# Kernel tuning notes

Hardware: AMD Instinct MI355X
Metric: run time of the kernel (lower is better)

## Reference

```python
import jax, jax.numpy as jnp
import numpy as np

N = 100000        # nodes
E = 1600000       # directed edges (before self loops)
F = 128           # input node features
H1, H2, H3 = 64, 32, 16
G = 64            # graphs in batch
EPS = 1e-5
NEG_SLOPE = 0.2


def setup_inputs():
    key = jax.random.key(0)
    ks = jax.random.split(key, 16)
    def rn(k, shape, scale=1.0):
        return jax.random.normal(k, shape, dtype=jnp.float32) * scale
    inp = {}
    inp['x'] = rn(ks[0], (N, F))
    inp['edge_index'] = jax.random.randint(ks[1], (2, E), 0, N)
    inp['batch'] = jnp.sort(jax.random.randint(ks[2], (N,), 0, G))
    dims = [(F, H1), (H1, H2), (H2, H3)]
    i = 3
    for li, (fi, fo) in enumerate(dims, start=1):
        s = 1.0 / np.sqrt(fi)
        kk = jax.random.split(ks[i], 3)
        inp[f'Wl{li}'] = rn(kk[0], (fi, fo), s)
        inp[f'bl{li}'] = jnp.zeros((fo,), jnp.float32)
        inp[f'Wr{li}'] = rn(kk[1], (fi, fo), s)
        inp[f'br{li}'] = jnp.zeros((fo,), jnp.float32)
        inp[f'att{li}'] = rn(kk[2], (fo,), 1.0 / np.sqrt(fo))
        inp[f'bias{li}'] = jnp.zeros((fo,), jnp.float32)
        inp[f'gamma{li}'] = jnp.ones((fo,), jnp.float32)
        inp[f'beta{li}'] = jnp.zeros((fo,), jnp.float32)
        i += 1
    inp['linW'] = rn(ks[i], (H3, 1), 0.25)
    inp['linb'] = jnp.zeros((1,), jnp.float32)
    return inp


def _gatv2(x, Wl, bl, Wr, br, att, bias, src, dst):
    # PyG GATv2Conv, heads=1: e_ij = a^T LeakyReLU(Wl x_j + Wr x_i)
    xl = x @ Wl + bl                         # [N, H] source transform
    xr = x @ Wr + br                         # [N, H] target transform
    e = jax.nn.leaky_relu(xl[src] + xr[dst], NEG_SLOPE) @ att   # [E']
    # numerically stable segment softmax over incoming edges of dst
    emax = jax.ops.segment_max(e, dst, num_segments=N)
    w = jnp.exp(e - emax[dst])
    denom = jax.ops.segment_sum(w, dst, num_segments=N)
    alpha = w / (denom[dst] + 1e-16)         # [E']
    out = jax.ops.segment_sum(alpha[:, None] * xl[src], dst, num_segments=N)
    return out + bias


def _batchnorm(x, gamma, beta):
    mu = jnp.mean(x, axis=0)
    var = jnp.var(x, axis=0)
    return (x - mu) * jax.lax.rsqrt(var + EPS) * gamma + beta


def reference(x, edge_index, batch,
              Wl1, bl1, Wr1, br1, att1, bias1, gamma1, beta1,
              Wl2, bl2, Wr2, br2, att2, bias2, gamma2, beta2,
              Wl3, bl3, Wr3, br3, att3, bias3, gamma3, beta3,
              linW, linb):
    # add self loops once (PyG GATv2Conv default add_self_loops=True)
    loops = jnp.arange(N, dtype=edge_index.dtype)
    src = jnp.concatenate([edge_index[0], loops])
    dst = jnp.concatenate([edge_index[1], loops])

    h = _gatv2(x, Wl1, bl1, Wr1, br1, att1, bias1, src, dst)
    h = jax.nn.relu(_batchnorm(h, gamma1, beta1))
    h = _gatv2(h, Wl2, bl2, Wr2, br2, att2, bias2, src, dst)
    h = jax.nn.relu(_batchnorm(h, gamma2, beta2))
    h = _gatv2(h, Wl3, bl3, Wr3, br3, att3, bias3, src, dst)
    h = jax.nn.relu(_batchnorm(h, gamma3, beta3))

    # global mean pool over graphs
    sums = jax.ops.segment_sum(h, batch, num_segments=G)          # [G, 16]
    cnts = jax.ops.segment_sum(jnp.ones((N,), h.dtype), batch, num_segments=G)
    pooled = sums / jnp.maximum(cnts, 1.0)[:, None]
    return pooled @ linW + linb                                   # [G, 1]
```

## Files before the change

### kernel.cpp

```cpp
#include <hip/hip_runtime.h>
#include <hip/hip_bf16.h>


static constexpr int G_ = 64;

__global__ __launch_bounds__(256) void pack_w(
    const float* __restrict__ Wl, const float* __restrict__ Wr,
    const float* __restrict__ bl, const float* __restrict__ br,
    float* __restrict__ Wcat, float* __restrict__ bcat, int FI, int H) {
  int i = blockIdx.x * 256 + threadIdx.x;
  int FO = 2 * H;
  if (i < FI * FO) {
    int k = i / FO, c = i % FO;
    Wcat[i] = (c < H) ? Wl[k * H + c] : Wr[k * H + (c - H)];
  }
  if (i < FO) bcat[i] = (i < H) ? bl[i] : br[i - H];
}

template <int FI>
__global__ __launch_bounds__(256) void transpose_nf(
    const float* __restrict__ A, float* __restrict__ At, int N) {
  __shared__ float s[64][65];
  int n0 = blockIdx.x * 64, k0 = blockIdx.y * 64;
  int tid = threadIdx.x;
  for (int idx = tid; idx < 64 * 16; idx += 256) {
    int n = idx >> 4, c = idx & 15;
    float4 v = make_float4(0.f, 0.f, 0.f, 0.f);
    if (n0 + n < N)
      v = *reinterpret_cast<const float4*>(&A[(size_t)(n0 + n) * FI + k0 + c * 4]);
    s[n][c * 4 + 0] = v.x; s[n][c * 4 + 1] = v.y;
    s[n][c * 4 + 2] = v.z; s[n][c * 4 + 3] = v.w;
  }
  __syncthreads();
  for (int idx = tid; idx < 64 * 16; idx += 256) {
    int k = idx >> 4, c = idx & 15;
    int n = c * 4;
    if (n0 + n + 3 < N) {
      float4 v = make_float4(s[n][k], s[n + 1][k], s[n + 2][k], s[n + 3][k]);
      *reinterpret_cast<float4*>(&At[(size_t)(k0 + k) * N + n0 + n]) = v;
    } else {
      for (int j = 0; j < 4; j++)
        if (n0 + n + j < N) At[(size_t)(k0 + k) * N + n0 + n + j] = s[n + j][k];
    }
  }
}

__global__ __launch_bounds__(256) void edge_hist(
    const int* __restrict__ ei, int* __restrict__ deg, int E, int Etot, int N) {
  int p = blockIdx.x & 7;
  int q = blockIdx.x >> 3;
  int nbq = gridDim.x >> 3;
  float scale = 8.0f / (float)N;
  for (int i = q * 256 + threadIdx.x; i < Etot; i += nbq * 256) {
    int dst = (i < E) ? ei[E + i] : (i - E);
    int pp = min((int)((float)dst * scale), 7);
    if (pp == p) atomicAdd(&deg[dst], 1);
  }
}

__global__ __launch_bounds__(256) void scan1(
    const int* __restrict__ deg, int* __restrict__ part, int* __restrict__ bsums, int n) {
  __shared__ int ts[256];
  int t = threadIdx.x, b = blockIdx.x;
  int base = b * 1024 + t * 4;
  int d[4];
#pragma unroll
  for (int q = 0; q < 4; q++) d[q] = (base + q < n) ? deg[base + q] : 0;
  int s = d[0] + d[1] + d[2] + d[3];
  ts[t] = s;
  __syncthreads();
  for (int o = 1; o < 256; o <<= 1) {
    int v = (t >= o) ? ts[t - o] : 0;
    __syncthreads();
    ts[t] += v;
    __syncthreads();
  }
  int incl = ts[t];
  if (t == 255) bsums[b] = incl;
  int run = incl - s;
#pragma unroll
  for (int q = 0; q < 4; q++) {
    if (base + q < n) part[base + q] = run;
    run += d[q];
  }
}

__global__ void scan2(int* bsums, int nb) {
  if (threadIdx.x == 0 && blockIdx.x == 0) {
    int r = 0;
    for (int i = 0; i < nb; i++) { int t = bsums[i]; bsums[i] = r; r += t; }
  }
}

__global__ __launch_bounds__(256) void scan3(
    int* __restrict__ rp, int* __restrict__ cur, const int* __restrict__ bsums,
    int n, int Etot) {
  int i = blockIdx.x * 256 + threadIdx.x;
  if (i < n) {
    int v = rp[i] + bsums[i >> 10];
    rp[i] = v; cur[i] = v;
  }
  if (i == 0) rp[n] = Etot;
}

__global__ __launch_bounds__(256) void scatter_edges(
    const int* __restrict__ ei, int* __restrict__ cur, int* __restrict__ ssrc,
    int E, int Etot, int N) {
  int p = blockIdx.x & 7;
  int q = blockIdx.x >> 3;
  int nbq = gridDim.x >> 3;
  float scale = 8.0f / (float)N;
  for (int i = q * 256 + threadIdx.x; i < Etot; i += nbq * 256) {
    int dst = (i < E) ? ei[E + i] : (i - E);
    int pp = min((int)((float)dst * scale), 7);
    if (pp != p) continue;
    int src = (i < E) ? ei[i] : (i - E);
    int pos = atomicAdd(&cur[dst], 1);
    ssrc[pos] = src;
  }
}

template <int FI, int FO>
__global__ __launch_bounds__(256) void gemm_fmaj2(
    const float* __restrict__ At, const float* __restrict__ Wcat,
    const float* __restrict__ bcat, float* __restrict__ C, int N) {
  constexpr int KC = 32;
  constexpr int CT = FO / 16;
  __shared__ float As[KC * 128];
  __shared__ float Ws[KC * FO];
  int tid = threadIdx.x;
  int ng = tid & 15;
  int hg = tid >> 4;
  int n0 = blockIdx.x * 128;
  bool full = (n0 + 128 <= N);

  float acc[8][CT];
#pragma unroll
  for (int i = 0; i < 8; i++)
#pragma unroll
    for (int j = 0; j < CT; j++) acc[i][j] = 0.f;

  for (int kc = 0; kc < FI; kc += KC) {
    __syncthreads();
    {
      int r = tid >> 5;
      int c = (tid & 31) * 4;
      for (int rr = r; rr < KC; rr += 8) {
        float4 v;
        if (full) {
          v = *reinterpret_cast<const float4*>(&At[(size_t)(kc + rr) * N + n0 + c]);
        } else {
          float tmp[4];
#pragma unroll
          for (int j = 0; j < 4; j++)
            tmp[j] = (n0 + c + j < N) ? At[(size_t)(kc + rr) * N + n0 + c + j] : 0.f;
          v = make_float4(tmp[0], tmp[1], tmp[2], tmp[3]);
        }
        *reinterpret_cast<float4*>(&As[rr * 128 + c]) = v;
      }
    }
    for (int idx = tid; idx < KC * FO / 4; idx += 256)
      *reinterpret_cast<float4*>(&Ws[idx * 4]) =
          *reinterpret_cast<const float4*>(&Wcat[kc * FO + idx * 4]);
    __syncthreads();
#pragma unroll
    for (int kk = 0; kk < KC; kk++) {
      float4 alo = *reinterpret_cast<float4*>(&As[kk * 128 + 4 * ng]);
      float4 ahi = *reinterpret_cast<float4*>(&As[kk * 128 + 64 + 4 * ng]);
      float a[8] = {alo.x, alo.y, alo.z, alo.w, ahi.x, ahi.y, ahi.z, ahi.w};
      float w[CT];
#pragma unroll
      for (int j = 0; j < CT; j++) w[j] = Ws[kk * FO + hg * CT + j];
#pragma unroll
      for (int i = 0; i < 8; i++)
#pragma unroll
        for (int j = 0; j < CT; j++) acc[i][j] = fmaf(a[i], w[j], acc[i][j]);
    }
  }

  float b[CT];
#pragma unroll
  for (int j = 0; j < CT; j++) b[j] = bcat[hg * CT + j];
#pragma unroll
  for (int i = 0; i < 8; i++) {
    int n = n0 + ((i < 4) ? (4 * ng + i) : (64 + 4 * ng + (i - 4)));
    if (n < N) {
#pragma unroll
      for (int j = 0; j < CT; j++)
        C[(size_t)n * FO + hg * CT + j] = acc[i][j] + b[j];
    }
  }
}

__device__ __forceinline__ float lrelu02(float z) {
  return (z > 0.f) ? z : 0.2f * z;
}

template <int H, bool UN2>
__global__ __launch_bounds__(256) void gat_agg2(
    const float* __restrict__ xlr, const float* __restrict__ att,
    const float* __restrict__ bias, const int* __restrict__ rp,
    const int* __restrict__ ssrc, float* __restrict__ out, int N) {
  constexpr int L = H / 4;
  constexpr int C = 64 / L;
  int v = blockIdx.x * 4 + (threadIdx.x >> 6);
  if (v >= N) return;
  int lane = threadIdx.x & 63;
  int fl = lane % L;
  int sub = lane / L;

  const float4 xr4 = *reinterpret_cast<const float4*>(&xlr[(size_t)v * (2 * H) + H + fl * 4]);
  const float4 a4 = *reinterpret_cast<const float4*>(&att[fl * 4]);
  int beg = rp[v], end = rp[v + 1];

  float mA = -3.0e38f, dA = 0.f;
  float4 accA = make_float4(0.f, 0.f, 0.f, 0.f);
  float mB = -3.0e38f, dB = 0.f;
  float4 accB = make_float4(0.f, 0.f, 0.f, 0.f);

  constexpr int STEP = UN2 ? 2 * C : C;

  for (int j = beg + sub; j < end; j += STEP) {
    {
      int u = ssrc[j];
      float4 xl4 = *reinterpret_cast<const float4*>(&xlr[(size_t)u * (2 * H) + fl * 4]);
      float t = a4.x * lrelu02(xl4.x + xr4.x);
      t = fmaf(a4.y, lrelu02(xl4.y + xr4.y), t);
      t = fmaf(a4.z, lrelu02(xl4.z + xr4.z), t);
      t = fmaf(a4.w, lrelu02(xl4.w + xr4.w), t);
#pragma unroll
      for (int o = L / 2; o >= 1; o >>= 1) t += __shfl_xor(t, o);
      float diff = t - mA;
      if (diff > 8.f) {
        float sc = __expf(-diff);
        dA *= sc;
        accA.x *= sc; accA.y *= sc; accA.z *= sc; accA.w *= sc;
        mA = t; diff = 0.f;
      }
      float w = __expf(diff);
      dA += w;
      accA.x = fmaf(w, xl4.x, accA.x);
      accA.y = fmaf(w, xl4.y, accA.y);
      accA.z = fmaf(w, xl4.z, accA.z);
      accA.w = fmaf(w, xl4.w, accA.w);
    }
    if (UN2) {
      int j2 = j + C;
      if (j2 < end) {
        int u = ssrc[j2];
        float4 xl4 = *reinterpret_cast<const float4*>(&xlr[(size_t)u * (2 * H) + fl * 4]);
        float t = a4.x * lrelu02(xl4.x + xr4.x);
        t = fmaf(a4.y, lrelu02(xl4.y + xr4.y), t);
        t = fmaf(a4.z, lrelu02(xl4.z + xr4.z), t);
        t = fmaf(a4.w, lrelu02(xl4.w + xr4.w), t);
#pragma unroll
        for (int o = L / 2; o >= 1; o >>= 1) t += __shfl_xor(t, o);
        float diff = t - mB;
        if (diff > 8.f) {
          float sc = __expf(-diff);
          dB *= sc;
          accB.x *= sc; accB.y *= sc; accB.z *= sc; accB.w *= sc;
          mB = t; diff = 0.f;
        }
        float w = __expf(diff);
        dB += w;
        accB.x = fmaf(w, xl4.x, accB.x);
        accB.y = fmaf(w, xl4.y, accB.y);
        accB.z = fmaf(w, xl4.z, accB.z);
        accB.w = fmaf(w, xl4.w, accB.w);
      }
    }
  }

  if (UN2) {
    float mn = fmaxf(mA, mB);
    float s1 = __expf(mA - mn), s2 = __expf(mB - mn);
    dA = dA * s1 + dB * s2;
    accA.x = accA.x * s1 + accB.x * s2;
    accA.y = accA.y * s1 + accB.y * s2;
    accA.z = accA.z * s1 + accB.z * s2;
    accA.w = accA.w * s1 + accB.w * s2;
    mA = mn;
  }

#pragma unroll
  for (int o = L; o < 64; o <<= 1) {
    float mo = __shfl_xor(mA, o);
    float d2 = __shfl_xor(dA, o);
    float ax = __shfl_xor(accA.x, o);
    float ay = __shfl_xor(accA.y, o);
    float az = __shfl_xor(accA.z, o);
    float aw = __shfl_xor(accA.w, o);
    float mn = fmaxf(mA, mo);
    float s1 = __expf(mA - mn), s2 = __expf(mo - mn);
    dA = dA * s1 + d2 * s2;
    accA.x = accA.x * s1 + ax * s2;
    accA.y = accA.y * s1 + ay * s2;
    accA.z = accA.z * s1 + az * s2;
    accA.w = accA.w * s1 + aw * s2;
    mA = mn;
  }

  if (lane < L) {
    float inv = 1.f / (dA + 1e-16f);
    const float4 b4 = *reinterpret_cast<const float4*>(&bias[fl * 4]);
    float4 o4 = make_float4(fmaf(accA.x, inv, b4.x), fmaf(accA.y, inv, b4.y),
                            fmaf(accA.z, inv, b4.z), fmaf(accA.w, inv, b4.w));
    *reinterpret_cast<float4*>(&out[(size_t)v * H + fl * 4]) = o4;
  }
}

template <int H>
__global__ __launch_bounds__(256) void bn_stats(
    const float* __restrict__ X, float* __restrict__ stats, int N) {
  __shared__ float ls[256], ls2[256];
  int tid = threadIdx.x;
  int h = tid % H;
  constexpr int RPB = 256 / H;
  int r0 = blockIdx.x * RPB + tid / H;
  float s = 0.f, s2 = 0.f;
  for (int n = r0; n < N; n += gridDim.x * RPB) {
    float val = X[(size_t)n * H + h];
    s += val; s2 += val * val;
  }
  ls[tid] = s; ls2[tid] = s2;
  __syncthreads();
  if (tid < H) {
    for (int g = 1; g < RPB; g++) { s += ls[tid + g * H]; s2 += ls2[tid + g * H]; }
    atomicAdd(&stats[h], s);
    atomicAdd(&stats[H + h], s2);
  }
}

__global__ void bn_finalize(
    const float* __restrict__ stats, const float* __restrict__ gamma,
    const float* __restrict__ beta, float* __restrict__ ss, int H, int N) {
  int h = threadIdx.x;
  if (h < H) {
    float mean = stats[h] / (float)N;
    float var = stats[H + h] / (float)N - mean * mean;
    float istd = rsqrtf(var + 1e-5f);
    float sc = gamma[h] * istd;
    ss[h] = sc;
    ss[H + h] = beta[h] - mean * sc;
  }
}

template <int H>
__global__ __launch_bounds__(256) void bn_apply_T(
    const float* __restrict__ X, const float* __restrict__ ss,
    float* __restrict__ Yt, int N) {
  __shared__ float s[64][65];
  int n0 = blockIdx.x * 64;
  int tid = threadIdx.x;
  for (int idx = tid; idx < 64 * (H / 4); idx += 256) {
    int n = idx / (H / 4), c = idx % (H / 4);
    float4 v = make_float4(0.f, 0.f, 0.f, 0.f);
    if (n0 + n < N)
      v = *reinterpret_cast<const float4*>(&X[(size_t)(n0 + n) * H + c * 4]);
    s[n][c * 4 + 0] = v.x; s[n][c * 4 + 1] = v.y;
    s[n][c * 4 + 2] = v.z; s[n][c * 4 + 3] = v.w;
  }
  __syncthreads();
  for (int idx = tid; idx < H * 16; idx += 256) {
    int k = idx >> 4, c = idx & 15;
    int n = c * 4;
    float sc = ss[k], sh = ss[H + k];
    float t0 = s[n + 0][k] * sc + sh;
    float t1 = s[n + 1][k] * sc + sh;
    float t2 = s[n + 2][k] * sc + sh;
    float t3 = s[n + 3][k] * sc + sh;
    float4 v = make_float4(t0 > 0.f ? t0 : 0.f, t1 > 0.f ? t1 : 0.f,
                           t2 > 0.f ? t2 : 0.f, t3 > 0.f ? t3 : 0.f);
    if (n0 + n + 3 < N) {
      *reinterpret_cast<float4*>(&Yt[(size_t)k * N + n0 + n]) = v;
    } else {
      float tv[4] = {v.x, v.y, v.z, v.w};
      for (int j = 0; j < 4; j++)
        if (n0 + n + j < N) Yt[(size_t)k * N + n0 + n + j] = tv[j];
    }
  }
}

__global__ __launch_bounds__(256) void bn_apply_flat(
    const float* __restrict__ X, const float* __restrict__ ss,
    float* __restrict__ Y, int total) {
  int i = blockIdx.x * 256 + threadIdx.x;
  if (i < total) {
    int h = i & 15;
    float t = X[i] * ss[h] + ss[16 + h];
    Y[i] = t > 0.f ? t : 0.f;
  }
}

__global__ __launch_bounds__(256) void pool_kernel(
    const float* __restrict__ X, const int* __restrict__ batch,
    float* __restrict__ pool, float* __restrict__ cnt, int N) {
  __shared__ float lp[G_ * 16];
  __shared__ float lc[G_];
  int tid = threadIdx.x;
  for (int j = tid; j < G_ * 16; j += 256) lp[j] = 0.f;
  if (tid < G_) lc[tid] = 0.f;
  __syncthreads();
  int tot = N * 16;
  for (int i = blockIdx.x * 256 + tid; i < tot; i += gridDim.x * 256) {
    int n = i >> 4, h = i & 15;
    int g = batch[n];
    atomicAdd(&lp[g * 16 + h], X[i]);
    if (h == 0) atomicAdd(&lc[g], 1.0f);
  }
  __syncthreads();
  for (int j = tid; j < G_ * 16; j += 256) atomicAdd(&pool[j], lp[j]);
  if (tid < G_) atomicAdd(&cnt[tid], lc[tid]);
}

__global__ void final_linear(
    const float* __restrict__ pool, const float* __restrict__ cnt,
    const float* __restrict__ linW, const float* __restrict__ linb,
    float* __restrict__ out) {
  int g = threadIdx.x;
  if (g < G_) {
    float c = fmaxf(cnt[g], 1.0f);
    float acc = 0.f;
    for (int h = 0; h < 16; h++) acc += (pool[g * 16 + h] / c) * linW[h];
    out[g] = acc + linb[0];
  }
}

extern "C" void kernel_launch(void* const* d_in, const int* in_sizes, int n_in,
                              void* d_out, int out_size, void* d_ws, size_t ws_size,
                              hipStream_t stream) {
  const float* x = (const float*)d_in[0];
  const int* ei = (const int*)d_in[1];
  const int* batch = (const int*)d_in[2];
  const int N = in_sizes[0] / 128;
  const int E = in_sizes[1] / 2;
  const int Etot = E + N;

  char* wsb = (char*)d_ws;
  size_t off = 0;
  auto alloc = [&](size_t bytes) -> void* {
    void* p = wsb + off;
    off += (bytes + 255) & ~(size_t)255;
    return p;
  };
  float* R0 = (float*)alloc((size_t)128 * N * 4);
  float* R1 = (float*)alloc((size_t)128 * N * 4);
  float* R2 = (float*)alloc((size_t)64 * N * 4);
  int* deg = (int*)alloc((size_t)N * 4);
  int* row_ptr = (int*)alloc((size_t)(N + 1) * 4);
  int* cursor = (int*)alloc((size_t)N * 4);
  int* bsums = (int*)alloc(4096);
  int* ssrc = (int*)alloc((size_t)Etot * 4);
  float* Wc1 = (float*)alloc(16384 * 4);  float* bc1 = (float*)alloc(128 * 4);
  float* Wc2 = (float*)alloc(4096 * 4);   float* bc2 = (float*)alloc(64 * 4);
  float* Wc3 = (float*)alloc(1024 * 4);   float* bc3 = (float*)alloc(32 * 4);
  float* stats = (float*)alloc(128 * 4);
  float* ss = (float*)alloc(128 * 4);
  float* pool = (float*)alloc((G_ * 16 + G_) * 4);
  float* cnt = pool + G_ * 16;

  const float* Wl1 = (const float*)d_in[3];  const float* bl1 = (const float*)d_in[4];
  const float* Wr1 = (const float*)d_in[5];  const float* br1 = (const float*)d_in[6];
  const float* att1 = (const float*)d_in[7]; const float* bias1 = (const float*)d_in[8];
  const float* g1 = (const float*)d_in[9];   const float* b1 = (const float*)d_in[10];
  const float* Wl2 = (const float*)d_in[11]; const float* bl2 = (const float*)d_in[12];
  const float* Wr2 = (const float*)d_in[13]; const float* br2 = (const float*)d_in[14];
  const float* att2 = (const float*)d_in[15]; const float* bias2 = (const float*)d_in[16];
  const float* g2 = (const float*)d_in[17];  const float* b2 = (const float*)d_in[18];
  const float* Wl3 = (const float*)d_in[19]; const float* bl3 = (const float*)d_in[20];
  const float* Wr3 = (const float*)d_in[21]; const float* br3 = (const float*)d_in[22];
  const float* att3 = (const float*)d_in[23]; const float* bias3 = (const float*)d_in[24];
  const float* g3 = (const float*)d_in[25];  const float* b3 = (const float*)d_in[26];
  const float* linW = (const float*)d_in[27]; const float* linb = (const float*)d_in[28];
  float* out = (float*)d_out;

  int ntiles = (N + 63) / 64;
  int ntiles2 = (N + 127) / 128;
  int nb = (N + 1023) / 1024;
  int nnodeblk = (N + 3) / 4;

  pack_w<<<64, 256, 0, stream>>>(Wl1, Wr1, bl1, br1, Wc1, bc1, 128, 64);
  pack_w<<<16, 256, 0, stream>>>(Wl2, Wr2, bl2, br2, Wc2, bc2, 64, 32);
  pack_w<<<4, 256, 0, stream>>>(Wl3, Wr3, bl3, br3, Wc3, bc3, 32, 16);

  transpose_nf<128><<<dim3(ntiles, 2), 256, 0, stream>>>(x, R0, N);

  hipMemsetAsync(deg, 0, (size_t)N * 4, stream);
  edge_hist<<<4096, 256, 0, stream>>>(ei, deg, E, Etot, N);
  scan1<<<nb, 256, 0, stream>>>(deg, row_ptr, bsums, N);
  scan2<<<1, 64, 0, stream>>>(bsums, nb);
  scan3<<<(N + 255) / 256, 256, 0, stream>>>(row_ptr, cursor, bsums, N, Etot);
  scatter_edges<<<4096, 256, 0, stream>>>(ei, cursor, ssrc, E, Etot, N);

  gemm_fmaj2<128, 128><<<ntiles2, 256, 0, stream>>>(R0, Wc1, bc1, R1, N);
  gat_agg2<64, true><<<nnodeblk, 256, 0, stream>>>(R1, att1, bias1, row_ptr, ssrc, R2, N);
  hipMemsetAsync(stats, 0, 128 * 4, stream);
  bn_stats<64><<<512, 256, 0, stream>>>(R2, stats, N);
  bn_finalize<<<1, 64, 0, stream>>>(stats, g1, b1, ss, 64, N);
  bn_apply_T<64><<<ntiles, 256, 0, stream>>>(R2, ss, R0, N);

  gemm_fmaj2<64, 64><<<ntiles2, 256, 0, stream>>>(R0, Wc2, bc2, R1, N);
  gat_agg2<32, true><<<nnodeblk, 256, 0, stream>>>(R1, att2, bias2, row_ptr, ssrc, R2, N);
  hipMemsetAsync(stats, 0, 128 * 4, stream);
  bn_stats<32><<<512, 256, 0, stream>>>(R2, stats, N);
  bn_finalize<<<1, 64, 0, stream>>>(stats, g2, b2, ss, 32, N);
  bn_apply_T<32><<<ntiles, 256, 0, stream>>>(R2, ss, R0, N);

  gemm_fmaj2<32, 32><<<ntiles2, 256, 0, stream>>>(R0, Wc3, bc3, R1, N);
  gat_agg2<16, false><<<nnodeblk, 256, 0, stream>>>(R1, att3, bias3, row_ptr, ssrc, R2, N);
  hipMemsetAsync(stats, 0, 128 * 4, stream);
  bn_stats<16><<<512, 256, 0, stream>>>(R2, stats, N);
  bn_finalize<<<1, 64, 0, stream>>>(stats, g3, b3, ss, 16, N);
  bn_apply_flat<<<(N * 16 + 255) / 256, 256, 0, stream>>>(R2, ss, R0, N * 16);

  hipMemsetAsync(pool, 0, (G_ * 16 + G_) * 4, stream);
  pool_kernel<<<2048, 256, 0, stream>>>(R0, batch, pool, cnt, N);
  final_linear<<<1, 64, 0, stream>>>(pool, cnt, linW, linb, out);
}
```

Measured before the change: 603.7 us.

## Store GEMM outputs as bf16, fuse final BN into pool, merge launches

The GEMM now writes the concatenated xl/xr features as bf16 instead of fp32. This halves the bytes the edge-gather aggregation loads per neighbour, which is the dominant random-access traffic. The final BN-apply kernel is fused into the pooling kernel, and the three weight-pack kernels are merged into one. The memsets are combined into a single zeroing call, and the serial single-thread block-sum scan is replaced with a parallel shared-memory scan. Attention logits and aggregated features now carry bf16 rounding error, which could affect accuracy tolerance.

```diff
diff --git a/kernel.cpp b/kernel.cpp
--- a/kernel.cpp
+++ b/kernel.cpp
@@ -4,17 +4,38 @@
 
 static constexpr int G_ = 64;
 
-__global__ __launch_bounds__(256) void pack_w(
-    const float* __restrict__ Wl, const float* __restrict__ Wr,
-    const float* __restrict__ bl, const float* __restrict__ br,
-    float* __restrict__ Wcat, float* __restrict__ bcat, int FI, int H) {
+__device__ __forceinline__ float bf2f(unsigned short u) {
+  union { unsigned int i; float f; } c;
+  c.i = ((unsigned int)u) << 16;
+  return c.f;
+}
+__device__ __forceinline__ unsigned short f2bf(float f) {
+  union { float f; unsigned int i; } c;
+  c.f = f;
+  unsigned int r = c.i + 0x7FFFu + ((c.i >> 16) & 1u);
+  return (unsigned short)(r >> 16);
+}
+
+__global__ __launch_bounds__(256) void pack_all(
+    const float* __restrict__ Wl1, const float* __restrict__ Wr1,
+    const float* __restrict__ bl1, const float* __restrict__ br1,
+    const float* __restrict__ Wl2, const float* __restrict__ Wr2,
+    const float* __restrict__ bl2, const float* __restrict__ br2,
+    const float* __restrict__ Wl3, const float* __restrict__ Wr3,
+    const float* __restrict__ bl3, const float* __restrict__ br3,
+    float* __restrict__ Wc1, float* __restrict__ bc1,
+    float* __restrict__ Wc2, float* __restrict__ bc2,
+    float* __restrict__ Wc3, float* __restrict__ bc3) {
   int i = blockIdx.x * 256 + threadIdx.x;
-  int FO = 2 * H;
-  if (i < FI * FO) {
-    int k = i / FO, c = i % FO;
-    Wcat[i] = (c < H) ? Wl[k * H + c] : Wr[k * H + (c - H)];
-  }
-  if (i < FO) bcat[i] = (i < H) ? bl[i] : br[i - H];
+  if (i < 128 * 128) { int k = i >> 7, c = i & 127;
+    Wc1[i] = (c < 64) ? Wl1[k * 64 + c] : Wr1[k * 64 + c - 64]; }
+  if (i < 128) bc1[i] = (i < 64) ? bl1[i] : br1[i - 64];
+  if (i < 64 * 64) { int k = i >> 6, c = i & 63;
+    Wc2[i] = (c < 32) ? Wl2[k * 32 + c] : Wr2[k * 32 + c - 32]; }
+  if (i < 64) bc2[i] = (i < 32) ? bl2[i] : br2[i - 32];
+  if (i < 32 * 32) { int k = i >> 5, c = i & 31;
+    Wc3[i] = (c < 16) ? Wl3[k * 16 + c] : Wr3[k * 16 + c - 16]; }
+  if (i < 32) bc3[i] = (i < 16) ? bl3[i] : br3[i - 16];
 }
 
 template <int FI>
@@ -86,10 +107,18 @@
 }
 
 __global__ void scan2(int* bsums, int nb) {
-  if (threadIdx.x == 0 && blockIdx.x == 0) {
-    int r = 0;
-    for (int i = 0; i < nb; i++) { int t = bsums[i]; bsums[i] = r; r += t; }
-  }
+  __shared__ int s[256];
+  int t = threadIdx.x;
+  int v = (t < nb) ? bsums[t] : 0;
+  s[t] = v;
+  __syncthreads();
+  for (int o = 1; o < 256; o <<= 1) {
+    int u = (t >= o) ? s[t - o] : 0;
+    __syncthreads();
+    s[t] += u;
+    __syncthreads();
+  }
+  if (t < nb) bsums[t] = s[t] - v;
 }
 
 __global__ __launch_bounds__(256) void scan3(
@@ -123,7 +152,7 @@
 template <int FI, int FO>
 __global__ __launch_bounds__(256) void gemm_fmaj2(
     const float* __restrict__ At, const float* __restrict__ Wcat,
-    const float* __restrict__ bcat, float* __restrict__ C, int N) {
+    const float* __restrict__ bcat, unsigned short* __restrict__ Cb, int N) {
   constexpr int KC = 32;
   constexpr int CT = FO / 16;
   __shared__ float As[KC * 128];
@@ -185,9 +214,21 @@
   for (int i = 0; i < 8; i++) {
     int n = n0 + ((i < 4) ? (4 * ng + i) : (64 + 4 * ng + (i - 4)));
     if (n < N) {
-#pragma unroll
-      for (int j = 0; j < CT; j++)
-        C[(size_t)n * FO + hg * CT + j] = acc[i][j] + b[j];
+      unsigned int u[CT / 2];
+#pragma unroll
+      for (int j2 = 0; j2 < CT / 2; j2++) {
+        unsigned int lo = f2bf(acc[i][2 * j2] + b[2 * j2]);
+        unsigned int hi = f2bf(acc[i][2 * j2 + 1] + b[2 * j2 + 1]);
+        u[j2] = lo | (hi << 16);
+      }
+      unsigned short* dst = &Cb[(size_t)n * FO + hg * CT];
+      if constexpr (CT == 8) {
+        *reinterpret_cast<uint4*>(dst) = make_uint4(u[0], u[1], u[2], u[3]);
+      } else if constexpr (CT == 4) {
+        *reinterpret_cast<uint2*>(dst) = make_uint2(u[0], u[1]);
+      } else {
+        *reinterpret_cast<unsigned int*>(dst) = u[0];
+      }
     }
   }
 }
@@ -198,7 +239,7 @@
 
 template <int H, bool UN2>
 __global__ __launch_bounds__(256) void gat_agg2(
-    const float* __restrict__ xlr, const float* __restrict__ att,
+    const unsigned short* __restrict__ xlr, const float* __restrict__ att,
     const float* __restrict__ bias, const int* __restrict__ rp,
     const int* __restrict__ ssrc, float* __restrict__ out, int N) {
   constexpr int L = H / 4;
@@ -209,7 +250,8 @@
   int fl = lane % L;
   int sub = lane / L;
 
-  const float4 xr4 = *reinterpret_cast<const float4*>(&xlr[(size_t)v * (2 * H) + H + fl * 4]);
+  ushort4 qr = *reinterpret_cast<const ushort4*>(&xlr[(size_t)v * (2 * H) + H + fl * 4]);
+  float xr0 = bf2f(qr.x), xr1 = bf2f(qr.y), xr2 = bf2f(qr.z), xr3 = bf2f(qr.w);
   const float4 a4 = *reinterpret_cast<const float4*>(&att[fl * 4]);
   int beg = rp[v], end = rp[v + 1];
 
@@ -223,11 +265,12 @@
   for (int j = beg + sub; j < end; j += STEP) {
     {
       int u = ssrc[j];
-      float4 xl4 = *reinterpret_cast<const float4*>(&xlr[(size_t)u * (2 * H) + fl * 4]);
-      float t = a4.x * lrelu02(xl4.x + xr4.x);
-      t = fmaf(a4.y, lrelu02(xl4.y + xr4.y), t);
-      t = fmaf(a4.z, lrelu02(xl4.z + xr4.z), t);
-      t = fmaf(a4.w, lrelu02(xl4.w + xr4.w), t);
+      ushort4 q = *reinterpret_cast<const ushort4*>(&xlr[(size_t)u * (2 * H) + fl * 4]);
+      float x0 = bf2f(q.x), x1 = bf2f(q.y), x2 = bf2f(q.z), x3 = bf2f(q.w);
+      float t = a4.x * lrelu02(x0 + xr0);
+      t = fmaf(a4.y, lrelu02(x1 + xr1), t);
+      t = fmaf(a4.z, lrelu02(x2 + xr2), t);
+      t = fmaf(a4.w, lrelu02(x3 + xr3), t);
 #pragma unroll
       for (int o = L / 2; o >= 1; o >>= 1) t += __shfl_xor(t, o);
       float diff = t - mA;
@@ -239,20 +282,21 @@
       }
       float w = __expf(diff);
       dA += w;
-      accA.x = fmaf(w, xl4.x, accA.x);
-      accA.y = fmaf(w, xl4.y, accA.y);
-      accA.z = fmaf(w, xl4.z, accA.z);
-      accA.w = fmaf(w, xl4.w, accA.w);
+      accA.x = fmaf(w, x0, accA.x);
+      accA.y = fmaf(w, x1, accA.y);
+      accA.z = fmaf(w, x2, accA.z);
+      accA.w = fmaf(w, x3, accA.w);
     }
     if (UN2) {
       int j2 = j + C;
       if (j2 < end) {
         int u = ssrc[j2];
-        float4 xl4 = *reinterpret_cast<const float4*>(&xlr[(size_t)u * (2 * H) + fl * 4]);
-        float t = a4.x * lrelu02(xl4.x + xr4.x);
-        t = fmaf(a4.y, lrelu02(xl4.y + xr4.y), t);
-        t = fmaf(a4.z, lrelu02(xl4.z + xr4.z), t);
-        t = fmaf(a4.w, lrelu02(xl4.w + xr4.w), t);
+        ushort4 q = *reinterpret_cast<const ushort4*>(&xlr[(size_t)u * (2 * H) + fl * 4]);
+        float x0 = bf2f(q.x), x1 = bf2f(q.y), x2 = bf2f(q.z), x3 = bf2f(q.w);
+        float t = a4.x * lrelu02(x0 + xr0);
+        t = fmaf(a4.y, lrelu02(x1 + xr1), t);
+        t = fmaf(a4.z, lrelu02(x2 + xr2), t);
+        t = fmaf(a4.w, lrelu02(x3 + xr3), t);
 #pragma unroll
         for (int o = L / 2; o >= 1; o >>= 1) t += __shfl_xor(t, o);
         float diff = t - mB;
@@ -264,10 +308,10 @@
         }
         float w = __expf(diff);
         dB += w;
-        accB.x = fmaf(w, xl4.x, accB.x);
-        accB.y = fmaf(w, xl4.y, accB.y);
-        accB.z = fmaf(w, xl4.z, accB.z);
-        accB.w = fmaf(w, xl4.w, accB.w);
+        accB.x = fmaf(w, x0, accB.x);
+        accB.y = fmaf(w, x1, accB.y);
+        accB.z = fmaf(w, x2, accB.z);
+        accB.w = fmaf(w, x3, accB.w);
       }
     }
   }
@@ -382,20 +426,10 @@
   }
 }
 
-__global__ __launch_bounds__(256) void bn_apply_flat(
+__global__ __launch_bounds__(256) void pool_kernel(
     const float* __restrict__ X, const float* __restrict__ ss,
-    float* __restrict__ Y, int total) {
-  int i = blockIdx.x * 256 + threadIdx.x;
-  if (i < total) {
-    int h = i & 15;
-    float t = X[i] * ss[h] + ss[16 + h];
-    Y[i] = t > 0.f ? t : 0.f;
-  }
-}
-
-__global__ __launch_bounds__(256) void pool_kernel(
-    const float* __restrict__ X, const int* __restrict__ batch,
-    float* __restrict__ pool, float* __restrict__ cnt, int N) {
+    const int* __restrict__ batch, float* __restrict__ pool,
+    float* __restrict__ cnt, int N) {
   __shared__ float lp[G_ * 16];
   __shared__ float lc[G_];
   int tid = threadIdx.x;
@@ -406,7 +440,9 @@
   for (int i = blockIdx.x * 256 + tid; i < tot; i += gridDim.x * 256) {
     int n = i >> 4, h = i & 15;
     int g = batch[n];
-    atomicAdd(&lp[g * 16 + h], X[i]);
+    float t = X[i] * ss[h] + ss[16 + h];
+    t = (t > 0.f) ? t : 0.f;
+    atomicAdd(&lp[g * 16 + h], t);
     if (h == 0) atomicAdd(&lc[g], 1.0f);
   }
   __syncthreads();
@@ -445,9 +481,8 @@
     return p;
   };
   float* R0 = (float*)alloc((size_t)128 * N * 4);
-  float* R1 = (float*)alloc((size_t)128 * N * 4);
+  unsigned short* R1b = (unsigned short*)alloc((size_t)128 * N * 2);
   float* R2 = (float*)alloc((size_t)64 * N * 4);
-  int* deg = (int*)alloc((size_t)N * 4);
   int* row_ptr = (int*)alloc((size_t)(N + 1) * 4);
   int* cursor = (int*)alloc((size_t)N * 4);
   int* bsums = (int*)alloc(4096);
@@ -455,9 +490,14 @@
   float* Wc1 = (float*)alloc(16384 * 4);  float* bc1 = (float*)alloc(128 * 4);
   float* Wc2 = (float*)alloc(4096 * 4);   float* bc2 = (float*)alloc(64 * 4);
   float* Wc3 = (float*)alloc(1024 * 4);   float* bc3 = (float*)alloc(32 * 4);
-  float* stats = (float*)alloc(128 * 4);
   float* ss = (float*)alloc(128 * 4);
-  float* pool = (float*)alloc((G_ * 16 + G_) * 4);
+  size_t zelems = (size_t)N + 3 * 128 + G_ * 16 + G_;
+  char* zb = (char*)alloc(zelems * 4);
+  int* deg = (int*)zb;
+  float* stats1 = (float*)(zb + (size_t)N * 4);
+  float* stats2 = stats1 + 128;
+  float* stats3 = stats2 + 128;
+  float* pool = stats3 + 128;
   float* cnt = pool + G_ * 16;
 
   const float* Wl1 = (const float*)d_in[3];  const float* bl1 = (const float*)d_in[4];
@@ -480,41 +520,34 @@
   int nb = (N + 1023) / 1024;
   int nnodeblk = (N + 3) / 4;
 
-  pack_w<<<64, 256, 0, stream>>>(Wl1, Wr1, bl1, br1, Wc1, bc1, 128, 64);
-  pack_w<<<16, 256, 0, stream>>>(Wl2, Wr2, bl2, br2, Wc2, bc2, 64, 32);
-  pack_w<<<4, 256, 0, stream>>>(Wl3, Wr3, bl3, br3, Wc3, bc3, 32, 16);
-
+  pack_all<<<64, 256, 0, stream>>>(Wl1, Wr1, bl1, br1, Wl2, Wr2, bl2, br2,
+                                   Wl3, Wr3, bl3, br3, Wc1, bc1, Wc2, bc2, Wc3, bc3);
+  hipMemsetAsync(zb, 0, zelems * 4, stream);
   transpose_nf<128><<<dim3(ntiles, 2), 256, 0, stream>>>(x, R0, N);
 
-  hipMemsetAsync(deg, 0, (size_t)N * 4, stream);
   edge_hist<<<4096, 256, 0, stream>>>(ei, deg, E, Etot, N);
   scan1<<<nb, 256, 0, stream>>>(deg, row_ptr, bsums, N);
-  scan2<<<1, 64, 0, stream>>>(bsums, nb);
+  scan2<<<1, 256, 0, stream>>>(bsums, nb);
   scan3<<<(N + 255) / 256, 256, 0, stream>>>(row_ptr, cursor, bsums, N, Etot);
   scatter_edges<<<4096, 256, 0, stream>>>(ei, cursor, ssrc, E, Etot, N);
 
-  gemm_fmaj2<128, 128><<<ntiles2, 256, 0, stream>>>(R0, Wc1, bc1, R1, N);
-  gat_agg2<64, true><<<nnodeblk, 256, 0, stream>>>(R1, att1, bias1, row_ptr, ssrc, R2, N);
-  hipMemsetAsync(stats, 0, 128 * 4, stream);
-  bn_stats<64><<<512, 256, 0, stream>>>(R2, stats, N);
-  bn_finalize<<<1, 64, 0, stream>>>(stats, g1, b1, ss, 64, N);
+  gemm_fmaj2<128, 128><<<ntiles2, 256, 0, stream>>>(R0, Wc1, bc1, R1b, N);
+  gat_agg2<64, true><<<nnodeblk, 256, 0, stream>>>(R1b, att1, bias1, row_ptr, ssrc, R2, N);
+  bn_stats<64><<<512, 256, 0, stream>>>(R2, stats1, N);
+  bn_finalize<<<1, 64, 0, stream>>>(stats1, g1, b1, ss, 64, N);
   bn_apply_T<64><<<ntiles, 256, 0, stream>>>(R2, ss, R0, N);
 
-  gemm_fmaj2<64, 64><<<ntiles2, 256, 0, stream>>>(R0, Wc2, bc2, R1, N);
-  gat_agg2<32, true><<<nnodeblk, 256, 0, stream>>>(R1, att2, bias2, row_ptr, ssrc, R2, N);
-  hipMemsetAsync(stats, 0, 128 * 4, stream);
-  bn_stats<32><<<512, 256, 0, stream>>>(R2, stats, N);
-  bn_finalize<<<1, 64, 0, stream>>>(stats, g2, b2, ss, 32, N);
+  gemm_fmaj2<64, 64><<<ntiles2, 256, 0, stream>>>(R0, Wc2, bc2, R1b, N);
+  gat_agg2<32, true><<<nnodeblk, 256, 0, stream>>>(R1b, att2, bias2, row_ptr, ssrc, R2, N);
+  bn_stats<32><<<512, 256, 0, stream>>>(R2, stats2, N);
+  bn_finalize<<<1, 64, 0, stream>>>(stats2, g2, b2, ss, 32, N);
   bn_apply_T<32><<<ntiles, 256, 0, stream>>>(R2, ss, R0, N);
 
-  gemm_fmaj2<32, 32><<<ntiles2, 256, 0, stream>>>(R0, Wc3, bc3, R1, N);
-  gat_agg2<16, false><<<nnodeblk, 256, 0, stream>>>(R1, att3, bias3, row_ptr, ssrc, R2, N);
-  hipMemsetAsync(stats, 0, 128 * 4, stream);
-  bn_stats<16><<<512, 256, 0, stream>>>(R2, stats, N);
-  bn_finalize<<<1, 64, 0, stream>>>(stats, g3, b3, ss, 16, N);
-  bn_apply_flat<<<(N * 16 + 255) / 256, 256, 0, stream>>>(R2, ss, R0, N * 16);
-
-  hipMemsetAsync(pool, 0, (G_ * 16 + G_) * 4, stream);
-  pool_kernel<<<2048, 256, 0, stream>>>(R0, batch, pool, cnt, N);
+  gemm_fmaj2<32, 32><<<ntiles2, 256, 0, stream>>>(R0, Wc3, bc3, R1b, N);
+  gat_agg2<16, false><<<nnodeblk, 256, 0, stream>>>(R1b, att3, bias3, row_ptr, ssrc, R2, N);
+  bn_stats<16><<<512, 256, 0, stream>>>(R2, stats3, N);
+  bn_finalize<<<1, 64, 0, stream>>>(stats3, g3, b3, ss, 16, N);
+
+  pool_kernel<<<2048, 256, 0, stream>>>(R2, ss, batch, pool, cnt, N);
   final_linear<<<1, 64, 0, stream>>>(pool, cnt, linW, linb, out);
 }
```

Measured after the change: 579.6 us. 4.0% less time.
